# Optimization experiments

Measured on AMD Instinct MI355X. Metric: run time of the kernel, lower is better.

Reference implementation:

```python
import jax, jax.numpy as jnp
import numpy as np

N_NODES, T, C_IN, B = 207, 12, 4, 4
NT = N_NODES * T
D, H = 96, 4
HD = D // H
FF = 4 * D
ENC_L, DEC_L = 4, 1
N_MASK = int(NT * 0.75)
N_UNMASK = NT - N_MASK
MAX_NEIGH = 40
ATTN_SCALE = 1.0 / float(np.sqrt(HD))
SQRT_D = float(np.sqrt(D))


def _ln(x, g, b, eps=1e-5):
    m = jnp.mean(x, -1, keepdims=True)
    v = jnp.mean((x - m) ** 2, -1, keepdims=True)
    return (x - m) * jax.lax.rsqrt(v + eps) * g + b


def _transformer(x, attn_mask, layers):
    # x: [B, S, D]; attn_mask: [S, S] bool (True = disallowed) or None.
    x = x * SQRT_D  # nn.Transformer-style input scaling
    def step(h, p):
        aw, ab, W1, B1, W2, B2, LN = p
        Bq, S, _ = h.shape
        q = (h @ aw[0] + ab[0]).reshape(Bq, S, H, HD)
        k = (h @ aw[1] + ab[1]).reshape(Bq, S, H, HD)
        v = (h @ aw[2] + ab[2]).reshape(Bq, S, H, HD)
        scores = jnp.einsum('bqhd,bkhd->bhqk', q, k) * ATTN_SCALE
        if attn_mask is not None:
            scores = jnp.where(attn_mask, jnp.float32(-1e30), scores)
        probs = jax.nn.softmax(scores, axis=-1)
        o = jnp.einsum('bhqk,bkhd->bqhd', probs, v).reshape(Bq, S, D)
        h = _ln(h + o @ aw[3] + ab[3], LN[0, 0], LN[0, 1])  # post-norm (torch default)
        f = jax.nn.relu(h @ W1 + B1) @ W2 + B2
        h = _ln(h + f, LN[1, 0], LN[1, 1])
        return h, None
    x, _ = jax.lax.scan(step, x, layers)
    return x


def _layer_params(key, nlayers):
    ks = jax.random.split(key, 3)
    attn_w = jax.random.normal(ks[0], (nlayers, 4, D, D), jnp.float32) / float(np.sqrt(D))
    w1 = jax.random.normal(ks[1], (nlayers, D, FF), jnp.float32) / float(np.sqrt(D))
    w2 = jax.random.normal(ks[2], (nlayers, FF, D), jnp.float32) / float(np.sqrt(FF))
    ln = jnp.broadcast_to(jnp.stack([jnp.ones(D), jnp.zeros(D)]), (nlayers, 2, 2, D)).astype(jnp.float32)
    return (attn_w, jnp.zeros((nlayers, 4, D), jnp.float32), w1,
            jnp.zeros((nlayers, FF), jnp.float32), w2, jnp.zeros((nlayers, D), jnp.float32), ln)


def setup_inputs() -> dict:
    key = jax.random.key(0)
    ks = jax.random.split(key, 12)
    rng = np.random.default_rng(42)
    perm = rng.permutation(NT)
    masked_idx = jnp.asarray(np.sort(perm[:N_MASK]), jnp.int32)
    unmasked_idx = jnp.asarray(np.sort(perm[N_MASK:]), jnp.int32)
    ea = _layer_params(ks[3], ENC_L)
    da = _layer_params(ks[4], DEC_L)
    return dict(
        history_data=jax.random.uniform(ks[0], (B, T, N_NODES, C_IN), jnp.float32),
        unmasked_idx=unmasked_idx, masked_idx=masked_idx,
        nodevec1=jax.random.normal(ks[1], (N_NODES, 10), jnp.float32),
        nodevec2=jax.random.normal(ks[2], (10, N_NODES), jnp.float32),
        dim_w=jax.random.normal(ks[5], (1, D), jnp.float32),
        dim_b=jnp.zeros((D,), jnp.float32),
        pos_emb=jax.random.uniform(ks[6], (NT, D), jnp.float32, -0.02, 0.02),
        tod_w=jax.random.normal(ks[7], (1, D), jnp.float32) * 0.02,
        tod_b=jnp.zeros((D,), jnp.float32),
        dow_w=jax.random.normal(ks[8], (1, D), jnp.float32) * 0.02,
        dow_b=jnp.zeros((D,), jnp.float32),
        mask_token=jax.random.normal(ks[9], (D,), jnp.float32) * 0.02,
        enc_attn_w=ea[0], enc_attn_b=ea[1], enc_ffn_w1=ea[2], enc_ffn_b1=ea[3],
        enc_ffn_w2=ea[4], enc_ffn_b2=ea[5], enc_ln=ea[6],
        enc_norm_g=jnp.ones((D,), jnp.float32), enc_norm_b=jnp.zeros((D,), jnp.float32),
        e2d_w=jax.random.normal(ks[10], (D, D), jnp.float32) / float(np.sqrt(D)),
        e2d_b=jnp.zeros((D,), jnp.float32),
        dec_attn_w=da[0], dec_attn_b=da[1], dec_ffn_w1=da[2], dec_ffn_b1=da[3],
        dec_ffn_w2=da[4], dec_ffn_b2=da[5], dec_ln=da[6],
        dec_norm_g=jnp.ones((D,), jnp.float32), dec_norm_b=jnp.zeros((D,), jnp.float32),
        out_w=jax.random.normal(ks[11], (D, 1), jnp.float32) / float(np.sqrt(D)),
        out_b=jnp.zeros((1,), jnp.float32),
    )


def reference(history_data, unmasked_idx, masked_idx, nodevec1, nodevec2,
              dim_w, dim_b, pos_emb, tod_w, tod_b, dow_w, dow_b, mask_token,
              enc_attn_w, enc_attn_b, enc_ffn_w1, enc_ffn_b1, enc_ffn_w2, enc_ffn_b2, enc_ln,
              enc_norm_g, enc_norm_b, e2d_w, e2d_b,
              dec_attn_w, dec_attn_b, dec_ffn_w1, dec_ffn_b1, dec_ffn_w2, dec_ffn_b2, dec_ln,
              dec_norm_g, dec_norm_b, out_w, out_b):
    hist = jnp.transpose(history_data, (0, 2, 3, 1))  # [B, N, C, T]
    tod = hist[:, :, 3:4, :].reshape(B, NT, 1)
    dow = hist[:, :, 2:3, :].reshape(B, NT, 1)
    # --- adaptive graph: softmax(relu(v1 v2)), threshold + top-40, straight-through ---
    A = jax.nn.softmax(jax.nn.relu(nodevec1 @ nodevec2), axis=1)
    kth = -jnp.sort(-A, axis=1)[:, MAX_NEIGH:MAX_NEIGH + 1]  # (MAX_NEIGH+1)-th largest per row
    keep = jnp.logical_and(A > 1.0 / N_NODES, A > kth).astype(A.dtype)
    bin_mask = jax.lax.stop_gradient(keep - A) + A
    adpA = A * bin_mask
    adpA_full = jnp.repeat(jnp.repeat(adpA, T, axis=0), T, axis=1)  # [NT, NT] block structure
    # --- embed + positional/temporal encoding ---
    x = jnp.transpose(hist[:, :, 0:1, :], (0, 1, 3, 2)) @ dim_w + dim_b  # [B, N, T, D]
    token = x.reshape(B, NT, D) + pos_emb + (tod @ tod_w + tod_b) + (dow @ dow_w + dow_b)
    # --- encoder over unmasked tokens with graph-derived attention mask ---
    enc_in = token[:, unmasked_idx, :]
    A_sub = adpA_full[unmasked_idx][:, unmasked_idx]
    attn_mask = A_sub == 0  # ~A.bool(): True = disallowed
    h = _transformer(enc_in, attn_mask,
                     (enc_attn_w, enc_attn_b, enc_ffn_w1, enc_ffn_b1, enc_ffn_w2, enc_ffn_b2, enc_ln))
    h = _ln(h, enc_norm_g, enc_norm_b)
    # --- decoder ---
    h = h @ e2d_w + e2d_b
    h_masked = (mask_token[None, None, :] + pos_emb[masked_idx]
                + (tod[:, masked_idx] @ tod_w + tod_b)
                + (dow[:, masked_idx] @ dow_w + dow_b))  # [B, N_MASK, D]
    full = jnp.concatenate([h, h_masked], axis=1)  # [B, NT, D]
    full = _transformer(full, None,
                        (dec_attn_w, dec_attn_b, dec_ffn_w1, dec_ffn_b1, dec_ffn_w2, dec_ffn_b2, dec_ln))
    full = _ln(full, dec_norm_g, dec_norm_b)
    recon = full @ out_w + out_b  # [B, NT, 1]
    recon_masked = recon[:, N_UNMASK:, :]
    label = jnp.transpose(hist, (0, 1, 3, 2))[:, :, :, 0].reshape(B, NT, 1)
    label_masked = label[:, masked_idx, :]
    return recon_masked, label_masked
```

## Files before the change

### kernel.cpp

```cpp
#include <hip/hip_runtime.h>
#include <math.h>

#define N_NODES 207
#define T_STEPS 12
#define NT 2484
#define BQ 4
#define DIM 96
#define NH 4
#define HD 24
#define FFD 384
#define N_MASK 1863
#define N_UNMASK 621
#define MAX_NEIGH 40
#define ATTN_SCALE 0.20412414523193154f
#define SQRT_DF 9.797958971132712f
#define KT 256
#define NMW 20

static inline int cdiv(int a, int b) { return (a + b - 1) / b; }

__global__ __launch_bounds__(256) void adj_kernel(const float* __restrict__ nv1,
                                                  const float* __restrict__ nv2,
                                                  float* __restrict__ keep) {
    int r = blockIdx.x, t = threadIdx.x;
    __shared__ float a[N_NODES];
    __shared__ float red[256];
    __shared__ int   redi[256];
    __shared__ int   taken[N_NODES];
    __shared__ float v1[10];
    __shared__ float kth;
    if (t < 10) v1[t] = nv1[r * 10 + t];
    __syncthreads();
    if (t < N_NODES) {
        float s = 0.f;
#pragma unroll
        for (int c = 0; c < 10; ++c) s += v1[c] * nv2[c * N_NODES + t];
        a[t] = fmaxf(s, 0.f);
        taken[t] = 0;
    }
    __syncthreads();
    red[t] = (t < N_NODES) ? a[t] : -3e38f;
    __syncthreads();
    for (int s = 128; s > 0; s >>= 1) {
        if (t < s) red[t] = fmaxf(red[t], red[t + s]);
        __syncthreads();
    }
    float mx = red[0];
    __syncthreads();
    float e = 0.f;
    if (t < N_NODES) e = __expf(a[t] - mx);
    red[t] = e;
    __syncthreads();
    for (int s = 128; s > 0; s >>= 1) {
        if (t < s) red[t] += red[t + s];
        __syncthreads();
    }
    float inv = 1.f / red[0];
    __syncthreads();
    if (t < N_NODES) a[t] = e * inv;
    __syncthreads();
    for (int round = 0; round <= MAX_NEIGH; ++round) {
        red[t]  = (t < N_NODES && !taken[t]) ? a[t] : -1.f;
        redi[t] = t;
        __syncthreads();
        for (int s = 128; s > 0; s >>= 1) {
            if (t < s && red[t + s] > red[t]) { red[t] = red[t + s]; redi[t] = redi[t + s]; }
            __syncthreads();
        }
        if (t == 0) {
            taken[redi[0]] = 1;
            if (round == MAX_NEIGH) kth = red[0];
        }
        __syncthreads();
    }
    if (t < N_NODES) {
        float av = a[t];
        keep[r * N_NODES + t] = (av > (1.f / 207.f) && av > kth) ? 1.f : 0.f;
    }
}

__global__ void unnode_kernel(const int* __restrict__ uidx, int* __restrict__ unn) {
    int i = blockIdx.x * blockDim.x + threadIdx.x;
    if (i < N_UNMASK) unn[i] = uidx[i] / T_STEPS;
}

__global__ void maskbits_kernel(const float* __restrict__ keep, const int* __restrict__ unn,
                                unsigned int* __restrict__ mw) {
    int q = blockIdx.x;
    int w = threadIdx.x;
    if (w >= NMW) return;
    const float* krow = keep + unn[q] * N_NODES;
    unsigned int word = 0;
    for (int j = 0; j < 32; ++j) {
        int k = w * 32 + j;
        if (k < N_UNMASK && krow[unn[k]] != 0.f) word |= (1u << j);
    }
    mw[q * NMW + w] = word;
}

__global__ void encin_kernel(const float* __restrict__ hist, const int* __restrict__ uidx,
                             const float* __restrict__ dim_w, const float* __restrict__ dim_b,
                             const float* __restrict__ pos,
                             const float* __restrict__ tod_w, const float* __restrict__ tod_b,
                             const float* __restrict__ dow_w, const float* __restrict__ dow_b,
                             float* __restrict__ h) {
    int idx = blockIdx.x * blockDim.x + threadIdx.x;
    if (idx >= BQ * N_UNMASK * DIM) return;
    int d = idx % DIM;
    int q = (idx / DIM) % N_UNMASK;
    int b = idx / (DIM * N_UNMASK);
    int u = uidx[q];
    int n = u / T_STEPS, t = u % T_STEPS;
    const float* hp = hist + ((size_t)(b * T_STEPS + t) * N_NODES + n) * 4;
    float h0 = hp[0], dw = hp[2], td = hp[3];
    float val = h0 * dim_w[d] + dim_b[d] + pos[u * DIM + d]
              + td * tod_w[d] + tod_b[d] + dw * dow_w[d] + dow_b[d];
    h[idx] = val * SQRT_DF;
}

__global__ void hmasked_kernel(const float* __restrict__ hist, const int* __restrict__ midx,
                               const float* __restrict__ mask_token, const float* __restrict__ pos,
                               const float* __restrict__ tod_w, const float* __restrict__ tod_b,
                               const float* __restrict__ dow_w, const float* __restrict__ dow_b,
                               float* __restrict__ full) {
    int idx = blockIdx.x * blockDim.x + threadIdx.x;
    if (idx >= BQ * N_MASK * DIM) return;
    int d = idx % DIM;
    int j = (idx / DIM) % N_MASK;
    int b = idx / (DIM * N_MASK);
    int m = midx[j];
    int n = m / T_STEPS, t = m % T_STEPS;
    const float* hp = hist + ((size_t)(b * T_STEPS + t) * N_NODES + n) * 4;
    float dw = hp[2], td = hp[3];
    float val = mask_token[d] + pos[m * DIM + d]
              + td * tod_w[d] + tod_b[d] + dw * dow_w[d] + dow_b[d];
    full[((size_t)(b * NT) + N_UNMASK + j) * DIM + d] = val * SQRT_DF;
}

__global__ void label_kernel(const float* __restrict__ hist, const int* __restrict__ midx,
                             float* __restrict__ out) {
    int idx = blockIdx.x * blockDim.x + threadIdx.x;
    if (idx >= BQ * N_MASK) return;
    int j = idx % N_MASK;
    int b = idx / N_MASK;
    int m = midx[j];
    int n = m / T_STEPS, t = m % T_STEPS;
    out[BQ * N_MASK + idx] = hist[((size_t)(b * T_STEPS + t) * N_NODES + n) * 4 + 0];
}

#define ACCROW(accv, av)                                          \
    accv.x += av.x*w0.x + av.y*w1.x + av.z*w2.x + av.w*w3.x;      \
    accv.y += av.x*w0.y + av.y*w1.y + av.z*w2.y + av.w*w3.y;      \
    accv.z += av.x*w0.z + av.y*w1.z + av.z*w2.z + av.w*w3.z;      \
    accv.w += av.x*w0.w + av.y*w1.w + av.z*w2.w + av.w*w3.w;

template<int WMODE>
__global__ __launch_bounds__(256) void tgemm_kernel(const float* __restrict__ A,
                                                    const float* __restrict__ W,
                                                    const float* __restrict__ bias,
                                                    const float* __restrict__ res,
                                                    float* __restrict__ C,
                                                    int M, int N, int K, int gm,
                                                    int relu, float scale, int rmode) {
    __shared__ float As[64][100];
    __shared__ float Ws[96][64];
    int tid = threadIdx.x;
    int bm = blockIdx.x % gm;
    int bn = blockIdx.x / gm;
    int m0 = bm * 64, n0 = bn * 64;
    int tn4 = (tid & 15) * 4;
    int tm4 = (tid >> 4) * 4;
    float4 acc0 = {0,0,0,0}, acc1 = {0,0,0,0}, acc2 = {0,0,0,0}, acc3 = {0,0,0,0};

    for (int kc = 0; kc < K; kc += 96) {
        if (kc) __syncthreads();
#pragma unroll
        for (int i = 0; i < 6; ++i) {
            int f = i * 256 + tid;
            int r = f / 24, c4 = (f % 24) * 4;
            float4 v = {0,0,0,0};
            if (m0 + r < M) v = *(const float4*)(A + (size_t)(m0 + r) * K + kc + c4);
            *(float4*)&As[r][c4] = v;
        }
#pragma unroll
        for (int i = 0; i < 6; ++i) {
            int f = i * 256 + tid;
            int kr = f >> 4, n4 = (f & 15) * 4;
            int gn = n0 + n4;
            float4 v = {0,0,0,0};
            if (gn < N) {
                if (WMODE == 0) {
                    v = *(const float4*)(W + (size_t)(kc + kr) * N + gn);
                } else {
                    int gg = gn / 96, nc = gn - gg * 96;
                    v = *(const float4*)(W + (size_t)gg * 9216 + (kc + kr) * 96 + nc);
                }
            }
            *(float4*)&Ws[kr][n4] = v;
        }
        __syncthreads();
#pragma unroll 4
        for (int k = 0; k < 96; k += 4) {
            float4 a0 = *(const float4*)&As[tm4 + 0][k];
            float4 a1 = *(const float4*)&As[tm4 + 1][k];
            float4 a2 = *(const float4*)&As[tm4 + 2][k];
            float4 a3 = *(const float4*)&As[tm4 + 3][k];
            float4 w0 = *(const float4*)&Ws[k + 0][tn4];
            float4 w1 = *(const float4*)&Ws[k + 1][tn4];
            float4 w2 = *(const float4*)&Ws[k + 2][tn4];
            float4 w3 = *(const float4*)&Ws[k + 3][tn4];
            ACCROW(acc0, a0)
            ACCROW(acc1, a1)
            ACCROW(acc2, a2)
            ACCROW(acc3, a3)
        }
    }

    int gn = n0 + tn4;
    if (gn >= N) return;
    float4 bv = *(const float4*)(bias + gn);
    float4 av[4] = {acc0, acc1, acc2, acc3};
#pragma unroll
    for (int i = 0; i < 4; ++i) {
        int grow = m0 + tm4 + i;
        if (grow >= M) break;
        float4 acc = av[i];
        acc.x += bv.x; acc.y += bv.y; acc.z += bv.z; acc.w += bv.w;
        if (res) {
            int rr = grow;
            if (rmode) { int bb = grow / N_MASK; rr = bb * NT + N_UNMASK + (grow - bb * N_MASK); }
            float4 rv = *(const float4*)(res + (size_t)rr * N + gn);
            acc.x += rv.x; acc.y += rv.y; acc.z += rv.z; acc.w += rv.w;
        }
        if (relu) {
            acc.x = fmaxf(acc.x, 0.f); acc.y = fmaxf(acc.y, 0.f);
            acc.z = fmaxf(acc.z, 0.f); acc.w = fmaxf(acc.w, 0.f);
        }
        acc.x *= scale; acc.y *= scale; acc.z *= scale; acc.w *= scale;
        *(float4*)(C + (size_t)grow * N + gn) = acc;
    }
}

template<int QPL>
__global__ __launch_bounds__(256) void fattn_kernel(const float* __restrict__ Qp,
                                                    const float* __restrict__ Kp,
                                                    const float* __restrict__ Vp,
                                                    float* __restrict__ O,
                                                    const unsigned int* __restrict__ maskw,
                                                    int S, int Sq, int qoff,
                                                    int nqt, int rs) {
    __shared__ float smem[12288];
    float* Ks = smem;
    float* Vs = smem + 6144;

    int t = threadIdx.x;
    int w = t >> 6, lane = t & 63;
    int bid = blockIdx.x;
    int qt = bid % nqt;
    int hh = (bid / nqt) % NH;
    int b  = bid / (nqt * NH);

    float qr[QPL][HD];
    bool qvalid[QPL];
#pragma unroll
    for (int h = 0; h < QPL; ++h) {
        int qidx = qt * (64 * QPL) + h * 64 + lane;
        qvalid[h] = qidx < Sq;
        if (qvalid[h]) {
            const float* qp = Qp + ((size_t)(b * S + qoff + qidx)) * rs + hh * HD;
#pragma unroll
            for (int i = 0; i < 6; ++i) {
                float4 v = *(const float4*)(qp + i * 4);
                qr[h][i*4+0] = v.x; qr[h][i*4+1] = v.y;
                qr[h][i*4+2] = v.z; qr[h][i*4+3] = v.w;
            }
        } else {
#pragma unroll
            for (int d = 0; d < HD; ++d) qr[h][d] = 0.f;
        }
    }

    float m[QPL], l[QPL];
    float acc[QPL][HD];
#pragma unroll
    for (int h = 0; h < QPL; ++h) {
        m[h] = -1e30f; l[h] = 0.f;
#pragma unroll
        for (int d = 0; d < HD; ++d) acc[h][d] = 0.f;
    }

    int nchunk = (S + KT - 1) / KT;
    for (int c = 0; c < nchunk; ++c) {
        __syncthreads();
        int base_k = c * KT;
#pragma unroll
        for (int i = 0; i < 6; ++i) {
            int fi = i * 256 + t;
            int row = fi / 6, cc = fi - row * 6;
            int gk = base_k + row;
            float4 kv = {0,0,0,0};
            float4 vv = {0,0,0,0};
            if (gk < S) {
                size_t roff = ((size_t)(b * S + gk)) * rs + hh * HD + cc * 4;
                kv = *(const float4*)(Kp + roff);
                vv = *(const float4*)(Vp + roff);
            }
            *(float4*)(Ks + row * HD + cc * 4) = kv;
            *(float4*)(Vs + row * HD + cc * 4) = vv;
        }
        __syncthreads();

        unsigned int mw0 = ~0u, mw1 = ~0u;
        if (QPL == 1 && maskw) {
            int qidx = qt * 64 + lane;
            if (qidx < Sq) {
                int wi = c * 8 + w * 2;
                mw0 = (wi     < NMW) ? maskw[qidx * NMW + wi]     : 0u;
                mw1 = (wi + 1 < NMW) ? maskw[qidx * NMW + wi + 1] : 0u;
            }
        }

        for (int g = 0; g < 16; ++g) {
            float sgrp[QPL][4];
            float pv[QPL][4];
#pragma unroll
            for (int j = 0; j < 4; ++j) {
                int j2 = g * 4 + j;
                int kk = (w << 6) + j2;
                int gk = base_k + kk;
                const float4* kr = (const float4*)(Ks + kk * HD);
                float d0[QPL];
#pragma unroll
                for (int h = 0; h < QPL; ++h) d0[h] = 0.f;
#pragma unroll
                for (int i = 0; i < 6; ++i) {
                    float4 kv = kr[i];
#pragma unroll
                    for (int h = 0; h < QPL; ++h) {
                        d0[h] += qr[h][i*4+0]*kv.x + qr[h][i*4+1]*kv.y
                               + qr[h][i*4+2]*kv.z + qr[h][i*4+3]*kv.w;
                    }
                }
#pragma unroll
                for (int h = 0; h < QPL; ++h) {
                    float s = d0[h] * ATTN_SCALE;
                    if (QPL == 1 && maskw) {
                        unsigned int wsel = (j2 & 32) ? mw1 : mw0;
                        if (!((wsel >> (j2 & 31)) & 1u)) s = -1e30f;
                    }
                    if (gk >= S) s = -INFINITY;
                    sgrp[h][j] = s;
                }
            }
#pragma unroll
            for (int h = 0; h < QPL; ++h) {
                float gmx = fmaxf(fmaxf(sgrp[h][0], sgrp[h][1]),
                                  fmaxf(sgrp[h][2], sgrp[h][3]));
                if (gmx > m[h]) {
                    float f = __expf(m[h] - gmx);
                    l[h] *= f;
#pragma unroll
                    for (int d = 0; d < HD; ++d) acc[h][d] *= f;
                    m[h] = gmx;
                }
#pragma unroll
                for (int j = 0; j < 4; ++j) {
                    float p = __expf(sgrp[h][j] - m[h]);
                    pv[h][j] = p;
                    l[h] += p;
                }
            }
#pragma unroll
            for (int j = 0; j < 4; ++j) {
                int kk = (w << 6) + g * 4 + j;
                const float4* vr = (const float4*)(Vs + kk * HD);
#pragma unroll
                for (int i = 0; i < 6; ++i) {
                    float4 vv = vr[i];
#pragma unroll
                    for (int h = 0; h < QPL; ++h) {
                        acc[h][i*4+0] += pv[h][j]*vv.x;
                        acc[h][i*4+1] += pv[h][j]*vv.y;
                        acc[h][i*4+2] += pv[h][j]*vv.z;
                        acc[h][i*4+3] += pv[h][j]*vv.w;
                    }
                }
            }
        }
    }

#pragma unroll
    for (int h = 0; h < QPL; ++h) {
        __syncthreads();
        float* my = smem + (size_t)(w * 64 + lane) * 27;
        my[0] = m[h]; my[1] = l[h];
#pragma unroll
        for (int d = 0; d < HD; ++d) my[2 + d] = acc[h][d];
        __syncthreads();
        if (t < 64) {
            int qidx = qt * (64 * QPL) + h * 64 + t;
            if (qidx < Sq) {
                float M2 = -INFINITY;
#pragma unroll
                for (int w2 = 0; w2 < 4; ++w2)
                    M2 = fmaxf(M2, smem[(size_t)(w2 * 64 + t) * 27]);
                float L = 0.f;
                float o[HD];
#pragma unroll
                for (int d = 0; d < HD; ++d) o[d] = 0.f;
#pragma unroll
                for (int w2 = 0; w2 < 4; ++w2) {
                    const float* pp = smem + (size_t)(w2 * 64 + t) * 27;
                    float f = __expf(pp[0] - M2);
                    L += pp[1] * f;
#pragma unroll
                    for (int d = 0; d < HD; ++d) o[d] += pp[2 + d] * f;
                }
                float inv = 1.f / L;
                float* op = O + ((size_t)(b * Sq + qidx)) * DIM + hh * HD;
#pragma unroll
                for (int i = 0; i < 6; ++i) {
                    float4 v = make_float4(o[i*4+0] * inv, o[i*4+1] * inv,
                                           o[i*4+2] * inv, o[i*4+3] * inv);
                    *(float4*)(op + i * 4) = v;
                }
            }
        }
    }
}

__global__ __launch_bounds__(256) void ln_kernel(const float* __restrict__ X,
                                                 const float* __restrict__ g,
                                                 const float* __restrict__ bta,
                                                 float* __restrict__ Y, int M) {
    int row = blockIdx.x * 4 + (threadIdx.x >> 6);
    if (row >= M) return;
    int lane = threadIdx.x & 63;
    const float* x = X + (size_t)row * DIM;
    float x0 = x[lane];
    float x1 = (lane < 32) ? x[64 + lane] : 0.f;
    float s = x0 + x1;
#pragma unroll
    for (int o = 32; o; o >>= 1) s += __shfl_xor(s, o);
    float mean = s * (1.f / DIM);
    float d0 = x0 - mean;
    float d1 = (lane < 32) ? (x1 - mean) : 0.f;
    float v = d0 * d0 + d1 * d1;
#pragma unroll
    for (int o = 32; o; o >>= 1) v += __shfl_xor(v, o);
    float rs = rsqrtf(v * (1.f / DIM) + 1e-5f);
    float* y = Y + (size_t)row * DIM;
    y[lane] = d0 * rs * g[lane] + bta[lane];
    if (lane < 32) y[64 + lane] = d1 * rs * g[64 + lane] + bta[64 + lane];
}

__global__ __launch_bounds__(256) void tail_kernel(const float* __restrict__ X,
                                                   const float* __restrict__ g1,
                                                   const float* __restrict__ b1,
                                                   const float* __restrict__ g2,
                                                   const float* __restrict__ b2,
                                                   const float* __restrict__ ow,
                                                   const float* __restrict__ ob,
                                                   float* __restrict__ out, int Mtail) {
    int row = blockIdx.x * 4 + (threadIdx.x >> 6);
    if (row >= Mtail) return;
    int lane = threadIdx.x & 63;
    bool lo = lane < 32;
    const float* x = X + (size_t)row * DIM;
    float x0 = x[lane];
    float x1 = lo ? x[64 + lane] : 0.f;
    float s = x0 + x1;
#pragma unroll
    for (int o = 32; o; o >>= 1) s += __shfl_xor(s, o);
    float mean = s * (1.f / DIM);
    float d0 = x0 - mean;
    float d1 = lo ? (x1 - mean) : 0.f;
    float v = d0 * d0 + d1 * d1;
#pragma unroll
    for (int o = 32; o; o >>= 1) v += __shfl_xor(v, o);
    float rs = rsqrtf(v * (1.f / DIM) + 1e-5f);
    float y0 = d0 * rs * g1[lane] + b1[lane];
    float y1 = lo ? (d1 * rs * g1[64 + lane] + b1[64 + lane]) : 0.f;
    s = y0 + y1;
#pragma unroll
    for (int o = 32; o; o >>= 1) s += __shfl_xor(s, o);
    mean = s * (1.f / DIM);
    d0 = y0 - mean;
    d1 = lo ? (y1 - mean) : 0.f;
    v = d0 * d0 + d1 * d1;
#pragma unroll
    for (int o = 32; o; o >>= 1) v += __shfl_xor(v, o);
    rs = rsqrtf(v * (1.f / DIM) + 1e-5f);
    float z0 = d0 * rs * g2[lane] + b2[lane];
    float z1 = lo ? (d1 * rs * g2[64 + lane] + b2[64 + lane]) : 0.f;
    float a = z0 * ow[lane] + (lo ? z1 * ow[64 + lane] : 0.f);
#pragma unroll
    for (int o = 32; o; o >>= 1) a += __shfl_xor(a, o);
    if (lane == 0) out[row] = a + ob[0];
}

__global__ void copy_enc_kernel(const float* __restrict__ src, float* __restrict__ full) {
    int idx = blockIdx.x * blockDim.x + threadIdx.x;
    if (idx >= BQ * N_UNMASK * DIM) return;
    int d = idx % DIM;
    int q = (idx / DIM) % N_UNMASK;
    int b = idx / (DIM * N_UNMASK);
    full[((size_t)(b * NT) + q) * DIM + d] = src[idx];
}

extern "C" void kernel_launch(void* const* d_in, const int* in_sizes, int n_in,
                              void* d_out, int out_size, void* d_ws, size_t ws_size,
                              hipStream_t stream) {
    const float* hist   = (const float*)d_in[0];
    const int*   uidx   = (const int*)d_in[1];
    const int*   midx   = (const int*)d_in[2];
    const float* nv1    = (const float*)d_in[3];
    const float* nv2    = (const float*)d_in[4];
    const float* dim_w  = (const float*)d_in[5];
    const float* dim_b  = (const float*)d_in[6];
    const float* pos    = (const float*)d_in[7];
    const float* tod_w  = (const float*)d_in[8];
    const float* tod_b  = (const float*)d_in[9];
    const float* dow_w  = (const float*)d_in[10];
    const float* dow_b  = (const float*)d_in[11];
    const float* mtok   = (const float*)d_in[12];
    const float* eaw    = (const float*)d_in[13];
    const float* eab    = (const float*)d_in[14];
    const float* ew1    = (const float*)d_in[15];
    const float* eb1    = (const float*)d_in[16];
    const float* ew2    = (const float*)d_in[17];
    const float* eb2    = (const float*)d_in[18];
    const float* eln    = (const float*)d_in[19];
    const float* eng    = (const float*)d_in[20];
    const float* enb    = (const float*)d_in[21];
    const float* e2dw   = (const float*)d_in[22];
    const float* e2db   = (const float*)d_in[23];
    const float* daw    = (const float*)d_in[24];
    const float* dab    = (const float*)d_in[25];
    const float* dw1    = (const float*)d_in[26];
    const float* db1    = (const float*)d_in[27];
    const float* dw2    = (const float*)d_in[28];
    const float* db2    = (const float*)d_in[29];
    const float* dln    = (const float*)d_in[30];
    const float* dng    = (const float*)d_in[31];
    const float* dnb    = (const float*)d_in[32];
    const float* ow     = (const float*)d_in[33];
    const float* ob     = (const float*)d_in[34];

    float* ws = (float*)d_ws;
    float*        keep  = ws;
    int*          unn   = (int*)(ws + 43008);
    unsigned int* maskw = (unsigned int*)(ws + 44032);
    float* eh = ws + 56576;
    float* e1 = ws + 295040;
    float* e2 = ws + 1248896;
    float* et = ws + 1487360;
    float* fh = ws + 1725824;
    float* qf = ws + 2679680;
    float* dh = ws + 5541248;
    float* dt = ws + 6256640;

    float* outp = (float*)d_out;
    const int ME = BQ * N_UNMASK;
    const int MD = BQ * NT;
    const int MT = BQ * N_MASK;
    const int gmE = cdiv(ME, 64);
    const int gmD = cdiv(MD, 64);
    const int gmT = cdiv(MT, 64);

    adj_kernel<<<N_NODES, 256, 0, stream>>>(nv1, nv2, keep);
    unnode_kernel<<<cdiv(N_UNMASK, 256), 256, 0, stream>>>(uidx, unn);
    maskbits_kernel<<<N_UNMASK, 32, 0, stream>>>(keep, unn, maskw);
    encin_kernel<<<cdiv(ME * DIM, 256), 256, 0, stream>>>(
        hist, uidx, dim_w, dim_b, pos, tod_w, tod_b, dow_w, dow_b, eh);
    label_kernel<<<cdiv(MT, 256), 256, 0, stream>>>(hist, midx, outp);

    for (int l = 0; l < 4; ++l) {
        const float* aw = eaw + (size_t)l * 4 * DIM * DIM;
        const float* ab = eab + (size_t)l * 4 * DIM;
        tgemm_kernel<1><<<gmE * 5, 256, 0, stream>>>(
            eh, aw, ab, nullptr, e1, ME, 288, 96, gmE, 0, 1.f, 0);
        fattn_kernel<1><<<BQ * NH * 10, 256, 0, stream>>>(
            e1, e1 + 96, e1 + 192, e2, maskw, N_UNMASK, N_UNMASK, 0, 10, 288);
        tgemm_kernel<0><<<gmE * 2, 256, 0, stream>>>(
            e2, aw + 3 * DIM * DIM, ab + 3 * DIM, eh, et, ME, 96, 96, gmE, 0, 1.f, 0);
        ln_kernel<<<cdiv(ME, 4), 256, 0, stream>>>(
            et, eln + (size_t)(l * 4 + 0) * DIM, eln + (size_t)(l * 4 + 1) * DIM, eh, ME);
        tgemm_kernel<0><<<gmE * 6, 256, 0, stream>>>(
            eh, ew1 + (size_t)l * DIM * FFD, eb1 + (size_t)l * FFD, nullptr, e1,
            ME, FFD, 96, gmE, 1, 1.f, 0);
        tgemm_kernel<0><<<gmE * 2, 256, 0, stream>>>(
            e1, ew2 + (size_t)l * FFD * DIM, eb2 + (size_t)l * DIM, eh, et,
            ME, 96, FFD, gmE, 0, 1.f, 0);
        ln_kernel<<<cdiv(ME, 4), 256, 0, stream>>>(
            et, eln + (size_t)(l * 4 + 2) * DIM, eln + (size_t)(l * 4 + 3) * DIM, eh, ME);
    }
    ln_kernel<<<cdiv(ME, 4), 256, 0, stream>>>(eh, eng, enb, e2, ME);
    tgemm_kernel<0><<<gmE * 2, 256, 0, stream>>>(
        e2, e2dw, e2db, nullptr, et, ME, 96, 96, gmE, 0, SQRT_DF, 0);
    copy_enc_kernel<<<cdiv(ME * DIM, 256), 256, 0, stream>>>(et, fh);
    hmasked_kernel<<<cdiv(MT * DIM, 256), 256, 0, stream>>>(
        hist, midx, mtok, pos, tod_w, tod_b, dow_w, dow_b, fh);

    tgemm_kernel<1><<<gmD * 5, 256, 0, stream>>>(
        fh, daw, dab, nullptr, qf, MD, 288, 96, gmD, 0, 1.f, 0);
    fattn_kernel<1><<<BQ * NH * 30, 256, 0, stream>>>(
        qf, qf + 96, qf + 192, e1, nullptr, NT, N_MASK, N_UNMASK, 30, 288);
    tgemm_kernel<0><<<gmT * 2, 256, 0, stream>>>(
        e1, daw + 3 * DIM * DIM, dab + 3 * DIM, fh, dh, MT, 96, 96, gmT, 0, 1.f, 1);
    ln_kernel<<<cdiv(MT, 4), 256, 0, stream>>>(dh, dln + 0 * DIM, dln + 1 * DIM, dt, MT);
    tgemm_kernel<0><<<gmT * 6, 256, 0, stream>>>(
        dt, dw1, db1, nullptr, qf, MT, FFD, 96, gmT, 1, 1.f, 0);
    tgemm_kernel<0><<<gmT * 2, 256, 0, stream>>>(
        qf, dw2, db2, dt, dh, MT, 96, FFD, gmT, 0, 1.f, 0);
    tail_kernel<<<cdiv(MT, 4), 256, 0, stream>>>(
        dh, dln + 2 * DIM, dln + 3 * DIM, dng, dnb, ow, ob, outp, MT);
}
```

Before: 826.2 us.

## Split attention over key ranges with a separate log-sum-exp combine kernel

```diff
diff --git a/kernel.cpp b/kernel.cpp
--- a/kernel.cpp
+++ b/kernel.cpp
@@ -245,10 +245,12 @@
 __global__ __launch_bounds__(256) void fattn_kernel(const float* __restrict__ Qp,
                                                     const float* __restrict__ Kp,
                                                     const float* __restrict__ Vp,
-                                                    float* __restrict__ O,
+                                                    float* __restrict__ Pm,
+                                                    float* __restrict__ Pl,
+                                                    float* __restrict__ Pacc,
                                                     const unsigned int* __restrict__ maskw,
                                                     int S, int Sq, int qoff,
-                                                    int nqt, int rs) {
+                                                    int nqt, int NS, int rs) {
     __shared__ float smem[12288];
     float* Ks = smem;
     float* Vs = smem + 6144;
@@ -256,9 +258,10 @@
     int t = threadIdx.x;
     int w = t >> 6, lane = t & 63;
     int bid = blockIdx.x;
-    int qt = bid % nqt;
-    int hh = (bid / nqt) % NH;
-    int b  = bid / (nqt * NH);
+    int ns = bid % NS; int r1 = bid / NS;
+    int qt = r1 % nqt; r1 /= nqt;
+    int hh = r1 % NH;
+    int b  = r1 / NH;
 
     float qr[QPL][HD];
     bool qvalid[QPL];
@@ -289,8 +292,12 @@
         for (int d = 0; d < HD; ++d) acc[h][d] = 0.f;
     }
 
-    int nchunk = (S + KT - 1) / KT;
-    for (int c = 0; c < nchunk; ++c) {
+    int ntile = (S + KT - 1) / KT;
+    int tpn = (ntile + NS - 1) / NS;
+    int c0 = ns * tpn;
+    int c1 = min(c0 + tpn, ntile);
+
+    for (int c = c0; c < c1; ++c) {
         __syncthreads();
         int base_k = c * KT;
 #pragma unroll
@@ -416,17 +423,46 @@
 #pragma unroll
                     for (int d = 0; d < HD; ++d) o[d] += pp[2 + d] * f;
                 }
-                float inv = 1.f / L;
-                float* op = O + ((size_t)(b * Sq + qidx)) * DIM + hh * HD;
-#pragma unroll
-                for (int i = 0; i < 6; ++i) {
-                    float4 v = make_float4(o[i*4+0] * inv, o[i*4+1] * inv,
-                                           o[i*4+2] * inv, o[i*4+3] * inv);
-                    *(float4*)(op + i * 4) = v;
-                }
-            }
-        }
-    }
+                size_t pb = ((size_t)((b * NH + hh) * NS + ns)) * Sq + qidx;
+                Pm[pb] = M2;
+                Pl[pb] = L;
+                float* pa = Pacc + pb * 24;
+#pragma unroll
+                for (int i = 0; i < 6; ++i)
+                    *(float4*)(pa + i * 4) = make_float4(o[i*4+0], o[i*4+1],
+                                                         o[i*4+2], o[i*4+3]);
+            }
+        }
+    }
+}
+
+__global__ __launch_bounds__(256) void attn_combine_kernel(const float* __restrict__ Pm,
+                                                           const float* __restrict__ Pl,
+                                                           const float* __restrict__ Pacc,
+                                                           float* __restrict__ O,
+                                                           int Sq, int NS) {
+    int tid = blockIdx.x * 256 + threadIdx.x;
+    if (tid >= BQ * NH * Sq * 6) return;
+    int d4 = tid % 6;
+    int q  = (tid / 6) % Sq;
+    int bh = tid / (6 * Sq);
+    float M = -1e30f;
+    for (int ns = 0; ns < NS; ++ns)
+        M = fmaxf(M, Pm[((size_t)bh * NS + ns) * Sq + q]);
+    float L = 0.f;
+    float ax = 0.f, ay = 0.f, az = 0.f, aw = 0.f;
+    for (int ns = 0; ns < NS; ++ns) {
+        size_t pb = ((size_t)bh * NS + ns) * Sq + q;
+        float wgt = __expf(Pm[pb] - M);
+        L += wgt * Pl[pb];
+        float4 f0 = *(const float4*)(Pacc + pb * 24 + d4 * 4);
+        ax += wgt * f0.x; ay += wgt * f0.y;
+        az += wgt * f0.z; aw += wgt * f0.w;
+    }
+    float inv = 1.f / L;
+    int b = bh >> 2, hh = bh & 3;
+    float* op = O + ((size_t)(b * Sq + q)) * DIM + hh * HD + d4 * 4;
+    *(float4*)op = make_float4(ax * inv, ay * inv, az * inv, aw * inv);
 }
 
 __global__ __launch_bounds__(256) void ln_kernel(const float* __restrict__ X,
@@ -559,6 +595,13 @@
     float* qf = ws + 2679680;
     float* dh = ws + 5541248;
     float* dt = ws + 6256640;
+    float* PaccE = ws + 5541248;
+    float* PmE   = ws + 6256640;
+    float* PlE   = ws + 6286448;
+    float* PaccD = ws + 56576;
+    float* PmD   = ws + 1487360;
+    float* PlD   = ws + 1546976;
+    float* dLN = e1;
 
     float* outp = (float*)d_out;
     const int ME = BQ * N_UNMASK;
@@ -567,6 +610,9 @@
     const int gmE = cdiv(ME, 64);
     const int gmD = cdiv(MD, 64);
     const int gmT = cdiv(MT, 64);
+    const int NSE = 3, NSD = 2;
+    const int nqtE = 10;
+    const int nqtD = 15;
 
     adj_kernel<<<N_NODES, 256, 0, stream>>>(nv1, nv2, keep);
     unnode_kernel<<<cdiv(N_UNMASK, 256), 256, 0, stream>>>(uidx, unn);
@@ -580,8 +626,11 @@
         const float* ab = eab + (size_t)l * 4 * DIM;
         tgemm_kernel<1><<<gmE * 5, 256, 0, stream>>>(
             eh, aw, ab, nullptr, e1, ME, 288, 96, gmE, 0, 1.f, 0);
-        fattn_kernel<1><<<BQ * NH * 10, 256, 0, stream>>>(
-            e1, e1 + 96, e1 + 192, e2, maskw, N_UNMASK, N_UNMASK, 0, 10, 288);
+        fattn_kernel<1><<<BQ * NH * nqtE * NSE, 256, 0, stream>>>(
+            e1, e1 + 96, e1 + 192, PmE, PlE, PaccE, maskw,
+            N_UNMASK, N_UNMASK, 0, nqtE, NSE, 288);
+        attn_combine_kernel<<<cdiv(BQ * NH * N_UNMASK * 6, 256), 256, 0, stream>>>(
+            PmE, PlE, PaccE, e2, N_UNMASK, NSE);
         tgemm_kernel<0><<<gmE * 2, 256, 0, stream>>>(
             e2, aw + 3 * DIM * DIM, ab + 3 * DIM, eh, et, ME, 96, 96, gmE, 0, 1.f, 0);
         ln_kernel<<<cdiv(ME, 4), 256, 0, stream>>>(
@@ -604,15 +653,18 @@
 
     tgemm_kernel<1><<<gmD * 5, 256, 0, stream>>>(
         fh, daw, dab, nullptr, qf, MD, 288, 96, gmD, 0, 1.f, 0);
-    fattn_kernel<1><<<BQ * NH * 30, 256, 0, stream>>>(
-        qf, qf + 96, qf + 192, e1, nullptr, NT, N_MASK, N_UNMASK, 30, 288);
+    fattn_kernel<2><<<BQ * NH * nqtD * NSD, 256, 0, stream>>>(
+        qf, qf + 96, qf + 192, PmD, PlD, PaccD, nullptr,
+        NT, N_MASK, N_UNMASK, nqtD, NSD, 288);
+    attn_combine_kernel<<<cdiv(BQ * NH * N_MASK * 6, 256), 256, 0, stream>>>(
+        PmD, PlD, PaccD, dh, N_MASK, NSD);
     tgemm_kernel<0><<<gmT * 2, 256, 0, stream>>>(
-        e1, daw + 3 * DIM * DIM, dab + 3 * DIM, fh, dh, MT, 96, 96, gmT, 0, 1.f, 1);
-    ln_kernel<<<cdiv(MT, 4), 256, 0, stream>>>(dh, dln + 0 * DIM, dln + 1 * DIM, dt, MT);
+        dh, daw + 3 * DIM * DIM, dab + 3 * DIM, fh, dt, MT, 96, 96, gmT, 0, 1.f, 1);
+    ln_kernel<<<cdiv(MT, 4), 256, 0, stream>>>(dt, dln + 0 * DIM, dln + 1 * DIM, dLN, MT);
     tgemm_kernel<0><<<gmT * 6, 256, 0, stream>>>(
-        dt, dw1, db1, nullptr, qf, MT, FFD, 96, gmT, 1, 1.f, 0);
+        dLN, dw1, db1, nullptr, qf, MT, FFD, 96, gmT, 1, 1.f, 0);
     tgemm_kernel<0><<<gmT * 2, 256, 0, stream>>>(
-        qf, dw2, db2, dt, dh, MT, 96, FFD, gmT, 0, 1.f, 0);
+        qf, dw2, db2, dLN, dh, MT, 96, FFD, gmT, 0, 1.f, 0);
     tail_kernel<<<cdiv(MT, 4), 256, 0, stream>>>(
         dh, dln + 2 * DIM, dln + 3 * DIM, dng, dnb, ow, ob, outp, MT);
 }
```

After: 700.4 us. -15.2%, faster.
